# Kernel optimization log

Measured on AMD Instinct MI355X. Metric: run time of the kernel, lower is better.

Reference implementation:

```python
import jax, jax.numpy as jnp
import numpy as np

N_NODES = 100000
N_EDGES = 1600000
D_FEAT = 64
EPS_NORM = 1e-12  # torch F.normalize clamp


def setup_inputs() -> dict:
    key = jax.random.key(0)
    k1, k2, k3, k4 = jax.random.split(key, 4)
    x = jax.random.normal(k1, (N_NODES, D_FEAT), dtype=jnp.float32)
    row = jax.random.randint(k2, (N_EDGES,), 0, N_NODES, dtype=jnp.int32)
    offset = jax.random.randint(k3, (N_EDGES,), 1, N_NODES, dtype=jnp.int32)
    col = (row + offset) % N_NODES  # guarantees no self-loops
    edge_index = jnp.stack([row, col], axis=0)
    edge_attr = jax.random.uniform(k4, (N_EDGES,), dtype=jnp.float32)  # co-occurrence rates >= 0
    eps = jnp.zeros((1,), dtype=jnp.float32)
    beta = jnp.ones((1,), dtype=jnp.float32)
    return {"x": x, "edge_index": edge_index, "edge_attr": edge_attr, "eps": eps, "beta": beta}


def reference(x, edge_index, edge_attr, eps, beta):
    N, F = x.shape
    row, col = edge_index[0], edge_index[1]

    # Per-source-node L2 normalization of edge_attr (vectorized form of the
    # original python loop: edge_attr[row==i] = normalize(edge_attr[row==i], p=2))
    sq = jax.ops.segment_sum(edge_attr * edge_attr, row, num_segments=N)
    src_norm = jnp.maximum(jnp.sqrt(sq), EPS_NORM)
    ea = edge_attr / src_norm[row]

    # Add self loops with edge_attr = 1
    loop = jnp.arange(N, dtype=row.dtype)
    row2 = jnp.concatenate([row, loop])
    col2 = jnp.concatenate([col, loop])
    ea2 = jnp.concatenate([ea, jnp.ones((N,), dtype=ea.dtype)])

    # Row-wise L2 normalize node features
    xnorm = jnp.maximum(jnp.linalg.norm(x, axis=-1, keepdims=True), EPS_NORM)
    xn = x / xnorm

    # Segment softmax over edges grouped by source node (row)
    alpha = beta[0] * ea2
    amax = jax.ops.segment_max(alpha, row2, num_segments=N)
    e = jnp.exp(alpha - amax[row2])
    denom = jax.ops.segment_sum(e, row2, num_segments=N)
    alpha = e / denom[row2]

    # spmm: out[i] = sum_{(i,j) in E} alpha_ij * xn[j]
    out = jax.ops.segment_sum(alpha[:, None] * xn[col2], row2, num_segments=N)
    return (1.0 + eps[0]) * xn + out
```

## Files before the change

kernel.cpp:

```cpp
#include <hip/hip_runtime.h>
#include <math.h>

#define D 64
#define EPSN 1e-12f
#define RPB1 128
#define RPB1_SH 7
#define NBK_MAX 1024
#define CAPB 2560
#define CH 4096

__device__ __forceinline__ float bf2f(unsigned short u) {
    return __uint_as_float((unsigned)u << 16);
}
__device__ __forceinline__ unsigned short f2bf(float f) {
    unsigned u = __float_as_uint(f);
    u = (u + 0x7FFFu + ((u >> 16) & 1u)) >> 16;
    return (unsigned short)u;
}

__global__ __launch_bounds__(512) void k_xnp1(const int* __restrict__ row,
                                              const int* __restrict__ col,
                                              const float* __restrict__ ea,
                                              int* __restrict__ gcur1,
                                              float2* __restrict__ p1,
                                              const float4* __restrict__ x4,
                                              ushort4* __restrict__ xnh4,
                                              int E, int N, int p1b, int NBK1) {
    __shared__ unsigned hist[NBK_MAX];
    __shared__ unsigned gb[NBK_MAX];
    __shared__ unsigned loff[NBK_MAX];
    __shared__ unsigned lcur[NBK_MAX];
    __shared__ unsigned tmp[512];

    int tid = threadIdx.x;
    if ((int)blockIdx.x < p1b) {
        int base = blockIdx.x * CH;
        int end  = min(base + CH, E);

        hist[tid] = 0; hist[tid + 512] = 0;
        __syncthreads();

        for (int j = base + tid; j < end; j += 512)
            atomicAdd(&hist[(unsigned)row[j] >> RPB1_SH], 1u);
        __syncthreads();

        for (int i = tid; i < NBK1; i += 512) {
            unsigned c = hist[i];
            if (c) gb[i] = (unsigned)(i * CAPB) + (unsigned)atomicAdd(&gcur1[i], (int)c);
        }
        __syncthreads();

        unsigned a0 = hist[2 * tid], a1 = hist[2 * tid + 1];
        unsigned ts = a0 + a1;
        tmp[tid] = ts;
        __syncthreads();
        for (int off = 1; off < 512; off <<= 1) {
            unsigned add = (tid >= off) ? tmp[tid - off] : 0;
            __syncthreads();
            tmp[tid] += add;
            __syncthreads();
        }
        unsigned tb = tmp[tid] - ts;
        loff[2 * tid] = tb;
        loff[2 * tid + 1] = tb + a0;
        __syncthreads();
        lcur[tid] = loff[tid]; lcur[tid + 512] = loff[tid + 512];
        __syncthreads();

        for (int j = base + tid; j < end; j += 512) {
            unsigned r = (unsigned)row[j];
            unsigned b = r >> RPB1_SH;
            unsigned rank = atomicAdd(&lcur[b], 1u) - loff[b];
            unsigned gpos = gb[b] + rank;
            unsigned pk = ((r & (RPB1 - 1)) << 23) | (unsigned)col[j];
            p1[gpos] = make_float2(ea[j], __uint_as_float(pk));
        }
    } else {
        int t = (blockIdx.x - p1b) * 512 + tid;
        int r = t >> 4;
        int g = t & 15;
        if (r >= N) return;
        float4 v = x4[(size_t)r * 16 + g];
        float s = v.x * v.x + v.y * v.y + v.z * v.z + v.w * v.w;
        #pragma unroll
        for (int off = 8; off; off >>= 1) s += __shfl_xor(s, off);
        float inv = 1.0f / fmaxf(sqrtf(s), EPSN);
        ushort4 o;
        o.x = f2bf(v.x * inv); o.y = f2bf(v.y * inv);
        o.z = f2bf(v.z * inv); o.w = f2bf(v.w * inv);
        xnh4[(size_t)r * 16 + g] = o;
    }
}

template <int U>
__device__ __forceinline__ void gstep(const float2* __restrict__ lsrt, int k, unsigned lb,
                                      const char* __restrict__ xb,
                                      float& esum, float& acc) {
    float2 e[U];
    float xv[U];
    #pragma unroll
    for (int u = 0; u < U; ++u) e[u] = lsrt[k + u];
    #pragma unroll
    for (int u = 0; u < U; ++u)
        xv[u] = bf2f(*(const unsigned short*)(xb + (__float_as_uint(e[u].y) + lb)));
    #pragma unroll
    for (int u = 0; u < U; ++u) {
        esum += e[u].x;
        acc = fmaf(e[u].x, xv[u], acc);
    }
}

__global__ __launch_bounds__(512) void k_p2f(const int* __restrict__ gcnt,
                                             const float2* __restrict__ p1,
                                             const unsigned short* __restrict__ xnh,
                                             const float* __restrict__ beta,
                                             const float* __restrict__ eps,
                                             float* __restrict__ out, int N) {
    __shared__ float2   lsrt[CAPB];
    __shared__ float    lsq[RPB1];
    __shared__ unsigned ldeg[RPB1];
    __shared__ unsigned loff[RPB1];
    __shared__ unsigned lcur[RPB1];

    int b = blockIdx.x;
    int rowbase = b << RPB1_SH;
    int nrows = min(RPB1, N - rowbase);
    int s = b * CAPB;
    int cnt = gcnt[b];
    int tid = threadIdx.x;
    int wv = tid >> 6, lane = tid & 63;
    const char* xb = (const char*)xnh;
    unsigned lb = (unsigned)lane << 1;

    if (tid < RPB1) { ldeg[tid] = 0; lsq[tid] = 0.0f; }
    __syncthreads();

    for (int j = tid; j < cnt; j += 512) {
        float2 p = p1[s + j];
        unsigned rl = __float_as_uint(p.y) >> 23;
        atomicAdd(&ldeg[rl], 1u);
        atomicAdd(&lsq[rl], p.x * p.x);
    }
    __syncthreads();

    unsigned v = (tid < RPB1) ? ldeg[tid] : 0;
    if (tid < RPB1) loff[tid] = v;
    __syncthreads();
    for (int off = 1; off < RPB1; off <<= 1) {
        unsigned add = (tid < RPB1 && tid >= off) ? loff[tid - off] : 0;
        __syncthreads();
        if (tid < RPB1) loff[tid] += add;
        __syncthreads();
    }
    if (tid < RPB1) {
        unsigned ex = loff[tid] - v;
        loff[tid] = ex;
        lcur[tid] = ex;
        lsq[tid] = beta[0] / fmaxf(sqrtf(lsq[tid]), EPSN);
    }
    __syncthreads();

    for (int j = tid; j < cnt; j += 512) {
        float2 p = p1[s + j];
        unsigned pk = __float_as_uint(p.y);
        unsigned rl = pk >> 23;
        float w = __expf(p.x * lsq[rl]);
        unsigned pos = atomicAdd(&lcur[rl], 1u);
        lsrt[pos] = make_float2(w, __uint_as_float((pk & 0x7FFFFFu) << 7));
    }
    __syncthreads();

    float ebv = __expf(beta[0]);
    float c1 = 1.0f + eps[0];
    for (int r = wv; r < nrows; r += 8) {
        int ks = (int)loff[r];
        int ke = (r < RPB1 - 1) ? (int)loff[r + 1] : cnt;
        float esum = 0.0f, acc = 0.0f;
        int k = ks;
        for (; k + 16 <= ke; k += 16) gstep<16>(lsrt, k, lb, xb, esum, acc);
        if (k + 8 <= ke) { gstep<8>(lsrt, k, lb, xb, esum, acc); k += 8; }
        if (k + 4 <= ke) { gstep<4>(lsrt, k, lb, xb, esum, acc); k += 4; }
        for (; k < ke; ++k) {
            float2 e0 = lsrt[k];
            esum += e0.x;
            acc = fmaf(e0.x, bf2f(*(const unsigned short*)(xb + (__float_as_uint(e0.y) + lb))), acc);
        }
        int gr = rowbase + r;
        float xs = bf2f(*(const unsigned short*)(xb + (((unsigned)gr << 7) + lb)));
        float invden = 1.0f / (esum + ebv);
        out[((size_t)gr << 6) + lane] = c1 * xs + (acc + ebv * xs) * invden;
    }
}

static inline size_t align_up(size_t v, size_t a) { return (v + a - 1) & ~(a - 1); }

extern "C" void kernel_launch(void* const* d_in, const int* in_sizes, int n_in,
                              void* d_out, int out_size, void* d_ws, size_t ws_size,
                              hipStream_t stream) {
    const float* x    = (const float*)d_in[0];
    const int*   ei   = (const int*)d_in[1];
    const float* ea   = (const float*)d_in[2];
    const float* eps  = (const float*)d_in[3];
    const float* beta = (const float*)d_in[4];
    float* out = (float*)d_out;

    int N = in_sizes[0] / D;
    int E = in_sizes[2];
    const int* row = ei;
    const int* col = ei + E;
    int NBK1 = (N + RPB1 - 1) >> RPB1_SH;

    char* base = (char*)d_ws;
    size_t off = 0;
    unsigned short* xnh = (unsigned short*)(base + off); off = align_up(off + (size_t)N * D * sizeof(unsigned short), 256);
    int*    gcur1       = (int*)(base + off);            off = align_up(off + NBK_MAX * sizeof(int), 256);
    float2* p1buf       = (float2*)(base + off);

    hipMemsetAsync(gcur1, 0, NBK_MAX * sizeof(int), stream);

    int p1_blocks = (E + CH - 1) / CH;
    int xn_blocks = ((size_t)N * 16 + 511) / 512;

    k_xnp1<<<p1_blocks + xn_blocks, 512, 0, stream>>>(row, col, ea, gcur1, p1buf,
                                                      (const float4*)x, (ushort4*)xnh,
                                                      E, N, p1_blocks, NBK1);
    k_p2f <<<NBK1, 512, 0, stream>>>(gcur1, p1buf, xnh, beta, eps, out, N);
}
```

Before: 89.73 us.

## Split each row bucket of the fused gather kernel across four smaller blocks

The second kernel now launches four 256-thread blocks per 128-row bucket, each owning 32 rows. Each block scans the whole bucket, keeps only its own rows, and sorts them into a smaller LDS buffer. This raises block count and occupancy and cuts LDS use, so the gather over about 782 buckets balances better across CUs. The cost is that every block re-reads the full bucket from global memory. The new 768-entry cap also silently drops edges if a 32-row slice ever exceeds it.

Measured after the change: 96.93 us. +8.0%, slower.

```diff
diff --git a/kernel.cpp b/kernel.cpp
--- a/kernel.cpp
+++ b/kernel.cpp
@@ -8,6 +8,9 @@
 #define NBK_MAX 1024
 #define CAPB 2560
 #define CH 4096
+#define SUBSH 2
+#define SUBN (RPB1 >> SUBSH)
+#define CAPS 768
 
 __device__ __forceinline__ float bf2f(unsigned short u) {
     return __uint_as_float((unsigned)u << 16);
@@ -110,21 +113,25 @@
     }
 }
 
-__global__ __launch_bounds__(512) void k_p2f(const int* __restrict__ gcnt,
+__global__ __launch_bounds__(256) void k_p2f(const int* __restrict__ gcnt,
                                              const float2* __restrict__ p1,
                                              const unsigned short* __restrict__ xnh,
                                              const float* __restrict__ beta,
                                              const float* __restrict__ eps,
                                              float* __restrict__ out, int N) {
-    __shared__ float2   lsrt[CAPB];
-    __shared__ float    lsq[RPB1];
-    __shared__ unsigned ldeg[RPB1];
-    __shared__ unsigned loff[RPB1];
-    __shared__ unsigned lcur[RPB1];
-
-    int b = blockIdx.x;
-    int rowbase = b << RPB1_SH;
-    int nrows = min(RPB1, N - rowbase);
+    __shared__ float2   lsrt[CAPS];
+    __shared__ float    lsq[SUBN];
+    __shared__ unsigned ldeg[SUBN];
+    __shared__ unsigned loff[SUBN];
+    __shared__ unsigned lcur[SUBN];
+
+    int blk = blockIdx.x;
+    int b   = blk >> SUBSH;
+    int sub = blk & ((1 << SUBSH) - 1);
+    int rlbase  = sub * SUBN;
+    int rowbase = (b << RPB1_SH) + rlbase;
+    int nrows = min(SUBN, N - rowbase);
+    if (nrows <= 0) return;
     int s = b * CAPB;
     int cnt = gcnt[b];
     int tid = threadIdx.x;
@@ -132,27 +139,29 @@
     const char* xb = (const char*)xnh;
     unsigned lb = (unsigned)lane << 1;
 
-    if (tid < RPB1) { ldeg[tid] = 0; lsq[tid] = 0.0f; }
-    __syncthreads();
-
-    for (int j = tid; j < cnt; j += 512) {
+    if (tid < SUBN) { ldeg[tid] = 0; lsq[tid] = 0.0f; }
+    __syncthreads();
+
+    for (int j = tid; j < cnt; j += 256) {
         float2 p = p1[s + j];
-        unsigned rl = __float_as_uint(p.y) >> 23;
-        atomicAdd(&ldeg[rl], 1u);
-        atomicAdd(&lsq[rl], p.x * p.x);
-    }
-    __syncthreads();
-
-    unsigned v = (tid < RPB1) ? ldeg[tid] : 0;
-    if (tid < RPB1) loff[tid] = v;
-    __syncthreads();
-    for (int off = 1; off < RPB1; off <<= 1) {
-        unsigned add = (tid < RPB1 && tid >= off) ? loff[tid - off] : 0;
-        __syncthreads();
-        if (tid < RPB1) loff[tid] += add;
-        __syncthreads();
-    }
-    if (tid < RPB1) {
+        int rl = (int)(__float_as_uint(p.y) >> 23) - rlbase;
+        if ((unsigned)rl < (unsigned)SUBN) {
+            atomicAdd(&ldeg[rl], 1u);
+            atomicAdd(&lsq[rl], p.x * p.x);
+        }
+    }
+    __syncthreads();
+
+    unsigned v = (tid < SUBN) ? ldeg[tid] : 0;
+    if (tid < SUBN) loff[tid] = v;
+    __syncthreads();
+    for (int off = 1; off < SUBN; off <<= 1) {
+        unsigned add = (tid < SUBN && tid >= off) ? loff[tid - off] : 0;
+        __syncthreads();
+        if (tid < SUBN) loff[tid] += add;
+        __syncthreads();
+    }
+    if (tid < SUBN) {
         unsigned ex = loff[tid] - v;
         loff[tid] = ex;
         lcur[tid] = ex;
@@ -160,21 +169,23 @@
     }
     __syncthreads();
 
-    for (int j = tid; j < cnt; j += 512) {
+    for (int j = tid; j < cnt; j += 256) {
         float2 p = p1[s + j];
         unsigned pk = __float_as_uint(p.y);
-        unsigned rl = pk >> 23;
-        float w = __expf(p.x * lsq[rl]);
-        unsigned pos = atomicAdd(&lcur[rl], 1u);
-        lsrt[pos] = make_float2(w, __uint_as_float((pk & 0x7FFFFFu) << 7));
+        int rl = (int)(pk >> 23) - rlbase;
+        if ((unsigned)rl < (unsigned)SUBN) {
+            float w = __expf(p.x * lsq[rl]);
+            unsigned pos = atomicAdd(&lcur[rl], 1u);
+            if (pos < CAPS) lsrt[pos] = make_float2(w, __uint_as_float((pk & 0x7FFFFFu) << 7));
+        }
     }
     __syncthreads();
 
     float ebv = __expf(beta[0]);
     float c1 = 1.0f + eps[0];
-    for (int r = wv; r < nrows; r += 8) {
+    for (int r = wv; r < nrows; r += 4) {
         int ks = (int)loff[r];
-        int ke = (r < RPB1 - 1) ? (int)loff[r + 1] : cnt;
+        int ke = ks + (int)ldeg[r];
         float esum = 0.0f, acc = 0.0f;
         int k = ks;
         for (; k + 16 <= ke; k += 16) gstep<16>(lsrt, k, lb, xb, esum, acc);
@@ -224,5 +235,5 @@
     k_xnp1<<<p1_blocks + xn_blocks, 512, 0, stream>>>(row, col, ea, gcur1, p1buf,
                                                       (const float4*)x, (ushort4*)xnh,
                                                       E, N, p1_blocks, NBK1);
-    k_p2f <<<NBK1, 512, 0, stream>>>(gcur1, p1buf, xnh, beta, eps, out, N);
-}
+    k_p2f <<<NBK1 << SUBSH, 256, 0, stream>>>(gcur1, p1buf, xnh, beta, eps, out, N);
+}
```

## Halve rows per bucket, enlarge scatter chunks, pack degree and sum-of-squares atomics

Applied to the files above, without the earlier changes.

Halves rows per bucket to 64 (twice as many k_p2f blocks with half the shared staging each) and quadruples the edge chunk size per scatter block, giving fewer blocks and fewer global bucket-cursor atomics. The per-row degree count and squared-attribute sum now go into a single packed integer shared atomic, using fixed-point quantization of ea^2, instead of two separate atomics, one of them a float atomic. The fixed-point quantization introduces small rounding error in the normalization, and the 22-bit sum field could overflow for rows with very high degree. Bucket capacity is halved to match, which risks overflow if a bucket receives more than 1280 edges.

Result: slower. 92.16 us (+2.7%).

```diff
diff --git a/kernel.cpp b/kernel.cpp
--- a/kernel.cpp
+++ b/kernel.cpp
@@ -3,11 +3,11 @@
 
 #define D 64
 #define EPSN 1e-12f
-#define RPB1 128
-#define RPB1_SH 7
-#define NBK_MAX 1024
-#define CAPB 2560
-#define CH 4096
+#define RPB1 64
+#define RPB1_SH 6
+#define NBK_MAX 2048
+#define CAPB 1280
+#define CH 16384
 
 __device__ __forceinline__ float bf2f(unsigned short u) {
     return __uint_as_float((unsigned)u << 16);
@@ -37,7 +37,7 @@
         int base = blockIdx.x * CH;
         int end  = min(base + CH, E);
 
-        hist[tid] = 0; hist[tid + 512] = 0;
+        for (int i = tid; i < NBK_MAX; i += 512) hist[i] = 0;
         __syncthreads();
 
         for (int j = base + tid; j < end; j += 512)
@@ -50,8 +50,9 @@
         }
         __syncthreads();
 
-        unsigned a0 = hist[2 * tid], a1 = hist[2 * tid + 1];
-        unsigned ts = a0 + a1;
+        unsigned a0 = hist[4 * tid], a1 = hist[4 * tid + 1];
+        unsigned a2 = hist[4 * tid + 2], a3 = hist[4 * tid + 3];
+        unsigned ts = a0 + a1 + a2 + a3;
         tmp[tid] = ts;
         __syncthreads();
         for (int off = 1; off < 512; off <<= 1) {
@@ -61,10 +62,12 @@
             __syncthreads();
         }
         unsigned tb = tmp[tid] - ts;
-        loff[2 * tid] = tb;
-        loff[2 * tid + 1] = tb + a0;
-        __syncthreads();
-        lcur[tid] = loff[tid]; lcur[tid + 512] = loff[tid + 512];
+        loff[4 * tid] = tb;
+        loff[4 * tid + 1] = tb + a0;
+        loff[4 * tid + 2] = tb + a0 + a1;
+        loff[4 * tid + 3] = tb + a0 + a1 + a2;
+        __syncthreads();
+        for (int i = tid; i < NBK_MAX; i += 512) lcur[i] = loff[i];
         __syncthreads();
 
         for (int j = base + tid; j < end; j += 512) {
@@ -117,14 +120,16 @@
                                              const float* __restrict__ eps,
                                              float* __restrict__ out, int N) {
     __shared__ float2   lsrt[CAPB];
-    __shared__ float    lsq[RPB1];
+    __shared__ unsigned lpack[RPB1];
     __shared__ unsigned ldeg[RPB1];
     __shared__ unsigned loff[RPB1];
     __shared__ unsigned lcur[RPB1];
+    __shared__ float    lbinv[RPB1];
 
     int b = blockIdx.x;
     int rowbase = b << RPB1_SH;
     int nrows = min(RPB1, N - rowbase);
+    if (nrows <= 0) return;
     int s = b * CAPB;
     int cnt = gcnt[b];
     int tid = threadIdx.x;
@@ -132,19 +137,26 @@
     const char* xb = (const char*)xnh;
     unsigned lb = (unsigned)lane << 1;
 
-    if (tid < RPB1) { ldeg[tid] = 0; lsq[tid] = 0.0f; }
+    if (tid < RPB1) lpack[tid] = 0;
     __syncthreads();
 
     for (int j = tid; j < cnt; j += 512) {
         float2 p = p1[s + j];
         unsigned rl = __float_as_uint(p.y) >> 23;
-        atomicAdd(&ldeg[rl], 1u);
-        atomicAdd(&lsq[rl], p.x * p.x);
-    }
-    __syncthreads();
-
-    unsigned v = (tid < RPB1) ? ldeg[tid] : 0;
-    if (tid < RPB1) loff[tid] = v;
+        unsigned q = __float2uint_rn(p.x * p.x * 32768.0f);
+        atomicAdd(&lpack[rl], 0x400000u + q);
+    }
+    __syncthreads();
+
+    unsigned dv = 0;
+    if (tid < RPB1) {
+        unsigned pk = lpack[tid];
+        dv = pk >> 22;
+        ldeg[tid] = dv;
+        float sq = (float)(pk & 0x3FFFFFu) * (1.0f / 32768.0f);
+        lbinv[tid] = beta[0] / fmaxf(sqrtf(sq), EPSN);
+        loff[tid] = dv;
+    }
     __syncthreads();
     for (int off = 1; off < RPB1; off <<= 1) {
         unsigned add = (tid < RPB1 && tid >= off) ? loff[tid - off] : 0;
@@ -153,10 +165,9 @@
         __syncthreads();
     }
     if (tid < RPB1) {
-        unsigned ex = loff[tid] - v;
+        unsigned ex = loff[tid] - dv;
         loff[tid] = ex;
         lcur[tid] = ex;
-        lsq[tid] = beta[0] / fmaxf(sqrtf(lsq[tid]), EPSN);
     }
     __syncthreads();
 
@@ -164,7 +175,7 @@
         float2 p = p1[s + j];
         unsigned pk = __float_as_uint(p.y);
         unsigned rl = pk >> 23;
-        float w = __expf(p.x * lsq[rl]);
+        float w = __expf(p.x * lbinv[rl]);
         unsigned pos = atomicAdd(&lcur[rl], 1u);
         lsrt[pos] = make_float2(w, __uint_as_float((pk & 0x7FFFFFu) << 7));
     }
@@ -174,7 +185,7 @@
     float c1 = 1.0f + eps[0];
     for (int r = wv; r < nrows; r += 8) {
         int ks = (int)loff[r];
-        int ke = (r < RPB1 - 1) ? (int)loff[r + 1] : cnt;
+        int ke = ks + (int)ldeg[r];
         float esum = 0.0f, acc = 0.0f;
         int k = ks;
         for (; k + 16 <= ke; k += 16) gstep<16>(lsrt, k, lb, xb, esum, acc);
```
